# Performance work log

Measured on AMD Instinct MI355X. Metric: run time of the kernel, lower is better.

The kernel has to match this reference:

```python
import jax, jax.numpy as jnp
import numpy as np

N_HEAD, D_MODEL, D_K, D_V = 16, 1024, 64, 64
B, S = 2, 2048
LN_EPS = 1e-5


def setup_inputs() -> dict:
    key = jax.random.key(0)
    ks = jax.random.split(key, 9)
    std_qk = np.sqrt(2.0 / (D_MODEL + D_K)).astype(np.float32)
    std_v = np.sqrt(2.0 / (D_MODEL + D_V)).astype(np.float32)
    return {
        "q": jax.random.normal(ks[0], (B, S, D_MODEL), jnp.float32),
        "k": jax.random.normal(ks[1], (B, S, D_MODEL), jnp.float32),
        "v": jax.random.normal(ks[2], (B, S, D_MODEL), jnp.float32),
        # nn.Linear weights stored as [out, in]; we apply x @ W.T
        "w_qs": jax.random.normal(ks[3], (N_HEAD * D_K, D_MODEL), jnp.float32) * std_qk,
        "w_ks": jax.random.normal(ks[4], (N_HEAD * D_K, D_MODEL), jnp.float32) * std_qk,
        "w_vs": jax.random.normal(ks[5], (N_HEAD * D_V, D_MODEL), jnp.float32) * std_v,
        "fc_w": jax.random.normal(ks[6], (D_MODEL, N_HEAD * D_V), jnp.float32) * np.sqrt(2.0 / (D_MODEL + N_HEAD * D_V)).astype(np.float32),
        "fc_b": jnp.zeros((D_MODEL,), jnp.float32),
        "ln_g": jnp.ones((D_MODEL,), jnp.float32),
        "ln_b": jnp.zeros((D_MODEL,), jnp.float32),
    }


def reference(q, k, v, w_qs, w_ks, w_vs, fc_w, fc_b, ln_g, ln_b):
    temperature = jnp.asarray(np.power(D_K, 0.5), q.dtype)
    residual = q
    # projections -> [b, s, h, d]
    qh = (q @ w_qs.T).reshape(B, S, N_HEAD, D_K)
    kh = (k @ w_ks.T).reshape(B, S, N_HEAD, D_K)
    vh = (v @ w_vs.T).reshape(B, S, N_HEAD, D_V)
    # scaled dot-product attention (dropout = identity in eval)
    attn = jnp.einsum('bqhd,bkhd->bhqk', qh, kh) / temperature
    attn = jax.nn.softmax(attn, axis=-1)  # (log_softmax in source is unused)
    out = jnp.einsum('bhqk,bkhd->bqhd', attn, vh).reshape(B, S, N_HEAD * D_V)
    out = out @ fc_w.T + fc_b
    # layer norm over last dim
    x = out + residual
    mu = jnp.mean(x, axis=-1, keepdims=True)
    var = jnp.var(x, axis=-1, keepdims=True)
    return (x - mu) * jax.lax.rsqrt(var + LN_EPS) * ln_g + ln_b
```

## Files before the change

kernel.cpp:

```cpp
#include <hip/hip_runtime.h>
#include <hip/hip_bf16.h>

typedef _Float16 f16x8 __attribute__((ext_vector_type(8)));
typedef _Float16 f16x4 __attribute__((ext_vector_type(4)));
typedef _Float16 f16x2 __attribute__((ext_vector_type(2)));
typedef float f32x4 __attribute__((ext_vector_type(4)));

#define DEVI __device__ __forceinline__

constexpr int S_LEN = 2048;
constexpr int DM    = 1024;
constexpr int NH    = 16;
constexpr int DHD   = 64;
constexpr int MTOT  = 2 * S_LEN;

DEVI f32x4 mfma16(f16x8 a, f16x8 b, f32x4 c) {
    return __builtin_amdgcn_mfma_f32_16x16x32_f16(a, b, c, 0, 0, 0);
}

DEVI f16x2 cvt_pk(float a, float b) {
    return __builtin_bit_cast(f16x2, __builtin_amdgcn_cvt_pkrtz(a, b));
}

DEVI float fexp2(float x) {
#if __has_builtin(__builtin_amdgcn_exp2f)
    return __builtin_amdgcn_exp2f(x);
#else
    return exp2f(x);
#endif
}

__global__ void k_conv(const float* __restrict__ s0, const float* __restrict__ s1,
                       const float* __restrict__ s2, const float* __restrict__ s3,
                       const float* __restrict__ s4, const float* __restrict__ s5,
                       const float* __restrict__ s6,
                       _Float16* __restrict__ d0, _Float16* __restrict__ d1,
                       _Float16* __restrict__ d2, _Float16* __restrict__ d3,
                       _Float16* __restrict__ d4, _Float16* __restrict__ d5,
                       _Float16* __restrict__ d6)
{
    const int QN4 = (MTOT * DM) / 4;
    const int WN4 = (DM * DM) / 4;
    const int TOT = 3 * QN4 + 4 * WN4;
    int stride = gridDim.x * blockDim.x;
    for (int i = blockIdx.x * blockDim.x + threadIdx.x; i < TOT; i += stride) {
        const float* s; _Float16* d; int off;
        if (i < 3 * QN4) {
            int t = i / QN4; off = i - t * QN4;
            s = t == 0 ? s0 : (t == 1 ? s1 : s2);
            d = t == 0 ? d0 : (t == 1 ? d1 : d2);
        } else {
            int j = i - 3 * QN4;
            int t = j / WN4; off = j - t * WN4;
            s = t == 0 ? s3 : (t == 1 ? s4 : (t == 2 ? s5 : s6));
            d = t == 0 ? d3 : (t == 1 ? d4 : (t == 2 ? d5 : d6));
        }
        float4 v = reinterpret_cast<const float4*>(s)[off];
        f16x4 o;
        o[0] = (_Float16)v.x; o[1] = (_Float16)v.y;
        o[2] = (_Float16)v.z; o[3] = (_Float16)v.w;
        *reinterpret_cast<f16x4*>(d + (size_t)off * 4) = o;
    }
}

DEVI void gemm_main(const _Float16* __restrict__ A, const _Float16* __restrict__ Bw,
                    int kLen, int ld, int m0, int n0,
                    _Float16* As, _Float16* Bs, f32x4 (&acc)[4][4])
{
    const int tid = threadIdx.x;
    const int lane = tid & 63;
    const int w = tid >> 6;
    const int wm = w >> 1, wn = w & 1;
    const int lrow = lane & 15, lg = lane >> 4;
    const int srow = lane >> 3;
    const int sslot = lane & 7;

#pragma unroll
    for (int i = 0; i < 4; i++)
#pragma unroll
        for (int j = 0; j < 4; j++) acc[i][j] = f32x4{0.f, 0.f, 0.f, 0.f};

    f16x8 ra[4], rb[4];
#pragma unroll
    for (int q = 0; q < 4; q++) {
        int row = w * 8 + srow + q * 32;
        ra[q] = *reinterpret_cast<const f16x8*>(A  + (size_t)(m0 + row) * ld + sslot * 8);
        rb[q] = *reinterpret_cast<const f16x8*>(Bw + (size_t)(n0 + row) * ld + sslot * 8);
    }

    const int kTiles = kLen >> 6;
    for (int kt = 0; kt < kTiles; ++kt) {
        __syncthreads();
#pragma unroll
        for (int q = 0; q < 4; q++) {
            int row = w * 8 + srow + q * 32;
            int slot = sslot ^ (row & 7);
            *reinterpret_cast<f16x8*>(As + row * 64 + slot * 8) = ra[q];
            *reinterpret_cast<f16x8*>(Bs + row * 64 + slot * 8) = rb[q];
        }
        __syncthreads();
        if (kt + 1 < kTiles) {
#pragma unroll
            for (int q = 0; q < 4; q++) {
                int row = w * 8 + srow + q * 32;
                ra[q] = *reinterpret_cast<const f16x8*>(A  + (size_t)(m0 + row) * ld + (kt + 1) * 64 + sslot * 8);
                rb[q] = *reinterpret_cast<const f16x8*>(Bw + (size_t)(n0 + row) * ld + (kt + 1) * 64 + sslot * 8);
            }
        }
#pragma unroll
        for (int kk = 0; kk < 2; kk++) {
            f16x8 af[4], bfm[4];
#pragma unroll
            for (int i = 0; i < 4; i++) {
                int row = wm * 64 + i * 16 + lrow;
                int slot = (kk * 4 + lg) ^ (row & 7);
                af[i] = *reinterpret_cast<const f16x8*>(As + row * 64 + slot * 8);
            }
#pragma unroll
            for (int j = 0; j < 4; j++) {
                int row = wn * 64 + j * 16 + lrow;
                int slot = (kk * 4 + lg) ^ (row & 7);
                bfm[j] = *reinterpret_cast<const f16x8*>(Bs + row * 64 + slot * 8);
            }
#pragma unroll
            for (int i = 0; i < 4; i++)
#pragma unroll
                for (int j = 0; j < 4; j++)
                    acc[i][j] = mfma16(af[i], bfm[j], acc[i][j]);
        }
    }
}

__global__ __launch_bounds__(256, 2)
void k_proj(const _Float16* __restrict__ qb, const _Float16* __restrict__ kb,
            const _Float16* __restrict__ vb,
            const _Float16* __restrict__ wq, const _Float16* __restrict__ wk,
            const _Float16* __restrict__ wv,
            _Float16* __restrict__ Qh, _Float16* __restrict__ Kh, _Float16* __restrict__ Vt)
{
    __shared__ __align__(16) _Float16 As[128 * 64];
    __shared__ __align__(16) _Float16 Bs[128 * 64];
    const int z = blockIdx.z;
    const _Float16* A = z == 0 ? qb : (z == 1 ? kb : vb);
    const _Float16* B = z == 0 ? wq : (z == 1 ? wk : wv);
    const int m0 = blockIdx.x * 128, n0 = blockIdx.y * 128;
    f32x4 acc[4][4];
    gemm_main(A, B, DM, DM, m0, n0, As, Bs, acc);

    const int lane = threadIdx.x & 63, w = threadIdx.x >> 6;
    const int wm = w >> 1, wn = w & 1;
    const int lrow = lane & 15, lg = lane >> 4;

    if (z < 2) {
        _Float16* O = z == 0 ? Qh : Kh;
        const float scale = (z == 0) ? 0.18033688011112042f : 1.0f;
#pragma unroll
        for (int i = 0; i < 4; i++)
#pragma unroll
            for (int j = 0; j < 4; j++) {
                int n = n0 + wn * 64 + j * 16 + lrow;
                int h = n >> 6, d = n & 63;
#pragma unroll
                for (int r = 0; r < 4; r++) {
                    int m = m0 + wm * 64 + i * 16 + lg * 4 + r;
                    int b = m >> 11, s = m & (S_LEN - 1);
                    size_t idx = ((size_t)(b * NH + h) * S_LEN + s) * DHD + d;
                    O[idx] = (_Float16)(acc[i][j][r] * scale);
                }
            }
    } else {
#pragma unroll
        for (int i = 0; i < 4; i++) {
            int m = m0 + wm * 64 + i * 16 + lg * 4;
            int b = m >> 11, s = m & (S_LEN - 1);
#pragma unroll
            for (int j = 0; j < 4; j++) {
                int n = n0 + wn * 64 + j * 16 + lrow;
                int h = n >> 6, d = n & 63;
                size_t idx = ((size_t)(b * NH + h) * DHD + d) * S_LEN + s;
                f16x4 pk;
#pragma unroll
                for (int r = 0; r < 4; r++) pk[r] = (_Float16)acc[i][j][r];
                *reinterpret_cast<f16x4*>(Vt + idx) = pk;
            }
        }
    }
}

__global__ __launch_bounds__(256, 4)
void k_attn(const _Float16* __restrict__ Q, const _Float16* __restrict__ Kh,
            const _Float16* __restrict__ Vt, _Float16* __restrict__ Ob)
{
    __shared__ __align__(16) _Float16 Kl[2][64 * 64];
    __shared__ __align__(16) _Float16 Vl[2][64 * 64];
    __shared__ __align__(16) _Float16 Pl[4][16 * 64];

    const int tid  = threadIdx.x;
    const int lane = tid & 63, w = tid >> 6;
    const int lrow = lane & 15, lg = lane >> 4;

    const int raw  = blockIdx.x;
    const int swz  = (raw & 7) * 128 + (raw >> 3);
    const int bh   = swz >> 5;
    const int qblk = swz & 31;
    const int q0   = qblk * 64 + w * 16;

    const _Float16* Qb = Q  + (size_t)bh * S_LEN * DHD;
    const _Float16* Kb = Kh + (size_t)bh * S_LEN * DHD;
    const _Float16* Vb = Vt + (size_t)bh * DHD * S_LEN;

    f16x8 qf[2];
#pragma unroll
    for (int ks = 0; ks < 2; ks++)
        qf[ks] = *reinterpret_cast<const f16x8*>(Qb + (size_t)(q0 + lrow) * DHD + ks * 32 + lg * 8);

    f32x4 oacc[4];
#pragma unroll
    for (int df = 0; df < 4; df++) oacc[df] = f32x4{0.f, 0.f, 0.f, 0.f};
    f32x4 lacc = f32x4{0.f, 0.f, 0.f, 0.f};

    f16x8 vones;
#pragma unroll
    for (int i = 0; i < 8; i++) vones[i] = (_Float16)1.0f;

    const int srow8 = lane >> 3, sslot = lane & 7;
    const _Float16* gK = Kb + (size_t)(w * 16 + srow8) * DHD   + sslot * 8;
    const _Float16* gV = Vb + (size_t)(w * 16 + srow8) * S_LEN + sslot * 8;
    const int lds_st = (w * 16 + srow8) * 64 + (sslot ^ srow8) * 8;

    f16x8 stK[2], stV[2];
#pragma unroll
    for (int i = 0; i < 2; i++) {
        stK[i] = *reinterpret_cast<const f16x8*>(gK + i * 8 * DHD);
        stV[i] = *reinterpret_cast<const f16x8*>(gV + i * 8 * S_LEN);
    }

    for (int t = 0; t < 32; ++t) {
        const int cur = t & 1;
        _Float16* Kc = Kl[cur];
        _Float16* Vc = Vl[cur];
#pragma unroll
        for (int i = 0; i < 2; i++) {
            *reinterpret_cast<f16x8*>(Kc + lds_st + i * 8 * 64) = stK[i];
            *reinterpret_cast<f16x8*>(Vc + lds_st + i * 8 * 64) = stV[i];
        }
        if (t + 1 < 32) {
#pragma unroll
            for (int i = 0; i < 2; i++) {
                stK[i] = *reinterpret_cast<const f16x8*>(gK + (size_t)(t + 1) * 64 * DHD + i * 8 * DHD);
                stV[i] = *reinterpret_cast<const f16x8*>(gV + (t + 1) * 64 + i * 8 * S_LEN);
            }
        }
        asm volatile("s_waitcnt lgkmcnt(0)" ::: "memory");
        __builtin_amdgcn_s_barrier();

#pragma unroll
        for (int kf = 0; kf < 4; kf++) {
            const int r = kf * 16 + lrow;
            f16x8 k0 = *reinterpret_cast<const f16x8*>(Kc + r * 64 + ((lg    ) ^ (r & 7)) * 8);
            f16x8 k1 = *reinterpret_cast<const f16x8*>(Kc + r * 64 + ((4 + lg) ^ (r & 7)) * 8);
            __builtin_amdgcn_s_setprio(1);
            f32x4 sc = mfma16(k0, qf[0], f32x4{-7.f, -7.f, -7.f, -7.f});
            sc = mfma16(k1, qf[1], sc);
            __builtin_amdgcn_s_setprio(0);
            float p0 = fexp2(sc[0]), p1 = fexp2(sc[1]);
            float p2 = fexp2(sc[2]), p3 = fexp2(sc[3]);
            f16x4 hh = __builtin_shufflevector(cvt_pk(p0, p1), cvt_pk(p2, p3), 0, 1, 2, 3);
            const int sl = (kf * 2 + (lg >> 1)) ^ (lrow & 7);
            *reinterpret_cast<f16x4*>(&Pl[w][lrow * 64 + sl * 8 + (lg & 1) * 4]) = hh;
        }

#pragma unroll
        for (int ks = 0; ks < 2; ks++) {
            f16x8 pa = *reinterpret_cast<const f16x8*>(
                &Pl[w][lrow * 64 + ((ks * 4 + lg) ^ (lrow & 7)) * 8]);
            __builtin_amdgcn_s_setprio(1);
#pragma unroll
            for (int df = 0; df < 4; df++) {
                const int r = df * 16 + lrow;
                f16x8 vf = *reinterpret_cast<const f16x8*>(Vc + r * 64 + ((ks * 4 + lg) ^ (r & 7)) * 8);
                oacc[df] = mfma16(pa, vf, oacc[df]);
            }
            lacc = mfma16(pa, vones, lacc);
            __builtin_amdgcn_s_setprio(0);
        }
    }

    const int b = bh >> 4, h = bh & 15;
#pragma unroll
    for (int r = 0; r < 4; r++) {
        const float iq = 1.0f / lacc[r];
        const int m = b * S_LEN + q0 + lg * 4 + r;
#pragma unroll
        for (int df = 0; df < 4; df++)
            Ob[(size_t)m * DM + h * 64 + df * 16 + lrow] = (_Float16)(oacc[df][r] * iq);
    }
}

__global__ __launch_bounds__(256, 2)
void k_fc(const _Float16* __restrict__ Ob, const _Float16* __restrict__ Wfc,
          const float* __restrict__ bias,
          _Float16* __restrict__ fcoA, _Float16* __restrict__ fcoB)
{
    __shared__ __align__(16) _Float16 As[128 * 64];
    __shared__ __align__(16) _Float16 Bs[128 * 64];
    const int z = blockIdx.z;
    const int m0 = blockIdx.x * 128, n0 = blockIdx.y * 128;
    f32x4 acc[4][4];
    gemm_main(Ob + z * 512, Wfc + z * 512, 512, DM, m0, n0, As, Bs, acc);

    _Float16* out = z == 0 ? fcoA : fcoB;
    const int lane = threadIdx.x & 63, w = threadIdx.x >> 6;
    const int wm = w >> 1, wn = w & 1;
    const int lrow = lane & 15, lg = lane >> 4;
#pragma unroll
    for (int j = 0; j < 4; j++) {
        int n = n0 + wn * 64 + j * 16 + lrow;
        float bv = (z == 0) ? bias[n] : 0.f;
#pragma unroll
        for (int i = 0; i < 4; i++)
#pragma unroll
            for (int r = 0; r < 4; r++) {
                int m = m0 + wm * 64 + i * 16 + lg * 4 + r;
                out[(size_t)m * DM + n] = (_Float16)(acc[i][j][r] + bv);
            }
    }
}

__global__ void k_ln(const _Float16* __restrict__ fa, const _Float16* __restrict__ fb,
                     const float* __restrict__ res,
                     const float* __restrict__ g, const float* __restrict__ be,
                     float* __restrict__ out)
{
    int row = blockIdx.x * 4 + (threadIdx.x >> 6);
    int lane = threadIdx.x & 63;
    const f16x4* ar = reinterpret_cast<const f16x4*>(fa + (size_t)row * DM);
    const f16x4* br2 = reinterpret_cast<const f16x4*>(fb + (size_t)row * DM);
    const float4* rr = reinterpret_cast<const float4*>(res + (size_t)row * DM);
    float4 v[4];
    float sum = 0.f, sq = 0.f;
#pragma unroll
    for (int t = 0; t < 4; t++) {
        f16x4 a = ar[lane + 64 * t];
        f16x4 bq = br2[lane + 64 * t];
        float4 b = rr[lane + 64 * t];
        float4 c = make_float4((float)a[0] + (float)bq[0] + b.x,
                               (float)a[1] + (float)bq[1] + b.y,
                               (float)a[2] + (float)bq[2] + b.z,
                               (float)a[3] + (float)bq[3] + b.w);
        v[t] = c;
        sum += c.x + c.y + c.z + c.w;
        sq  += c.x * c.x + c.y * c.y + c.z * c.z + c.w * c.w;
    }
#pragma unroll
    for (int o = 1; o < 64; o <<= 1) { sum += __shfl_xor(sum, o); sq += __shfl_xor(sq, o); }
    float mu = sum * (1.f / DM);
    float rstd = rsqrtf(fmaxf(sq * (1.f / DM) - mu * mu, 0.f) + 1e-5f);
    float4* orow = reinterpret_cast<float4*>(out + (size_t)row * DM);
    const float4* gr = reinterpret_cast<const float4*>(g);
    const float4* brr = reinterpret_cast<const float4*>(be);
#pragma unroll
    for (int t = 0; t < 4; t++) {
        float4 gg = gr[lane + 64 * t], bb = brr[lane + 64 * t];
        float4 c = v[t];
        orow[lane + 64 * t] = make_float4((c.x - mu) * rstd * gg.x + bb.x,
                                          (c.y - mu) * rstd * gg.y + bb.y,
                                          (c.z - mu) * rstd * gg.z + bb.z,
                                          (c.w - mu) * rstd * gg.w + bb.w);
    }
}

extern "C" void kernel_launch(void* const* d_in, const int* in_sizes, int n_in,
                              void* d_out, int out_size, void* d_ws, size_t ws_size,
                              hipStream_t stream)
{
    const float* q    = (const float*)d_in[0];
    const float* k    = (const float*)d_in[1];
    const float* v    = (const float*)d_in[2];
    const float* w_qs = (const float*)d_in[3];
    const float* w_ks = (const float*)d_in[4];
    const float* w_vs = (const float*)d_in[5];
    const float* fc_w = (const float*)d_in[6];
    const float* fc_b = (const float*)d_in[7];
    const float* ln_g = (const float*)d_in[8];
    const float* ln_b = (const float*)d_in[9];
    float* out = (float*)d_out;

    if (ws_size < (size_t)67108864) return;

    _Float16* ws  = (_Float16*)d_ws;
    _Float16* qbf = ws;
    _Float16* kbf = qbf + 4194304;
    _Float16* vbf = kbf + 4194304;
    _Float16* wq  = vbf + 4194304;
    _Float16* wk  = wq + 1048576;
    _Float16* wv  = wk + 1048576;
    _Float16* wfc = wv + 1048576;
    _Float16* Qh  = wfc + 1048576;
    _Float16* Kh  = Qh + 4194304;
    _Float16* Vt  = Kh + 4194304;
    _Float16* Ob  = Vt + 4194304;
    _Float16* fcoA = qbf;
    _Float16* fcoB = kbf;

    k_conv<<<2048, 256, 0, stream>>>(q, k, v, w_qs, w_ks, w_vs, fc_w,
                                     qbf, kbf, vbf, wq, wk, wv, wfc);
    k_proj<<<dim3(32, 8, 3), 256, 0, stream>>>(qbf, kbf, vbf, wq, wk, wv, Qh, Kh, Vt);
    k_attn<<<1024, 256, 0, stream>>>(Qh, Kh, Vt, Ob);
    k_fc<<<dim3(32, 8, 2), 256, 0, stream>>>(Ob, wfc, fc_b, fcoA, fcoB);
    k_ln<<<1024, 256, 0, stream>>>(fcoA, fcoB, q, ln_g, ln_b, out);
}
```

Before: 134.1 us.

## Use direct global-to-LDS double-buffered GEMM loads and 32-row attention tiles per wave

The shared GEMM routine now loads tiles straight from global memory into LDS with global_load_lds, double-buffered, so it needs one barrier per k-step instead of staging through registers with two barriers. The XOR swizzle moves to the global address side. Attention now has each wave handle 32 query rows instead of 16, so every loaded K/V fragment feeds twice as many MFMAs. To fit this, the grid is halved and the occupancy hint is lowered. The changes add LDS and register pressure and rely on the barrier to wait for the async LDS loads to finish.

```diff
diff --git a/kernel.cpp b/kernel.cpp
--- a/kernel.cpp
+++ b/kernel.cpp
@@ -28,6 +28,12 @@
 #else
     return exp2f(x);
 #endif
+}
+
+DEVI void gload_lds16(const _Float16* g, _Float16* l) {
+    __builtin_amdgcn_global_load_lds(
+        (const __attribute__((address_space(1))) void*)g,
+        (__attribute__((address_space(3))) void*)l, 16, 0, 0);
 }
 
 __global__ void k_conv(const float* __restrict__ s0, const float* __restrict__ s1,
@@ -64,49 +70,47 @@
 }
 
 DEVI void gemm_main(const _Float16* __restrict__ A, const _Float16* __restrict__ Bw,
-                    int kLen, int ld, int m0, int n0,
-                    _Float16* As, _Float16* Bs, f32x4 (&acc)[4][4])
-{
+                    int kLen, int ld, int m0, int n0, f32x4 (&acc)[4][4])
+{
+    __shared__ __align__(16) _Float16 As[2][128 * 64];
+    __shared__ __align__(16) _Float16 Bs[2][128 * 64];
+
     const int tid = threadIdx.x;
     const int lane = tid & 63;
     const int w = tid >> 6;
     const int wm = w >> 1, wn = w & 1;
     const int lrow = lane & 15, lg = lane >> 4;
-    const int srow = lane >> 3;
-    const int sslot = lane & 7;
+    const int srow = w * 8 + (lane >> 3);
+    const int scol = ((lane & 7) ^ (srow & 7)) * 8;
 
 #pragma unroll
     for (int i = 0; i < 4; i++)
 #pragma unroll
         for (int j = 0; j < 4; j++) acc[i][j] = f32x4{0.f, 0.f, 0.f, 0.f};
 
-    f16x8 ra[4], rb[4];
+    const _Float16* gA = A  + (size_t)(m0 + srow) * ld + scol;
+    const _Float16* gB = Bw + (size_t)(n0 + srow) * ld + scol;
+
 #pragma unroll
     for (int q = 0; q < 4; q++) {
-        int row = w * 8 + srow + q * 32;
-        ra[q] = *reinterpret_cast<const f16x8*>(A  + (size_t)(m0 + row) * ld + sslot * 8);
-        rb[q] = *reinterpret_cast<const f16x8*>(Bw + (size_t)(n0 + row) * ld + sslot * 8);
+        gload_lds16(gA + (size_t)q * 32 * ld, &As[0][(w * 8 + q * 32) * 64]);
+        gload_lds16(gB + (size_t)q * 32 * ld, &Bs[0][(w * 8 + q * 32) * 64]);
     }
 
     const int kTiles = kLen >> 6;
     for (int kt = 0; kt < kTiles; ++kt) {
         __syncthreads();
-#pragma unroll
-        for (int q = 0; q < 4; q++) {
-            int row = w * 8 + srow + q * 32;
-            int slot = sslot ^ (row & 7);
-            *reinterpret_cast<f16x8*>(As + row * 64 + slot * 8) = ra[q];
-            *reinterpret_cast<f16x8*>(Bs + row * 64 + slot * 8) = rb[q];
-        }
-        __syncthreads();
         if (kt + 1 < kTiles) {
+            const int nb = (kt + 1) & 1;
+            const int ko = (kt + 1) * 64;
 #pragma unroll
             for (int q = 0; q < 4; q++) {
-                int row = w * 8 + srow + q * 32;
-                ra[q] = *reinterpret_cast<const f16x8*>(A  + (size_t)(m0 + row) * ld + (kt + 1) * 64 + sslot * 8);
-                rb[q] = *reinterpret_cast<const f16x8*>(Bw + (size_t)(n0 + row) * ld + (kt + 1) * 64 + sslot * 8);
-            }
-        }
+                gload_lds16(gA + ko + (size_t)q * 32 * ld, &As[nb][(w * 8 + q * 32) * 64]);
+                gload_lds16(gB + ko + (size_t)q * 32 * ld, &Bs[nb][(w * 8 + q * 32) * 64]);
+            }
+        }
+        const _Float16* Ab = As[kt & 1];
+        const _Float16* Bb = Bs[kt & 1];
 #pragma unroll
         for (int kk = 0; kk < 2; kk++) {
             f16x8 af[4], bfm[4];
@@ -114,13 +118,13 @@
             for (int i = 0; i < 4; i++) {
                 int row = wm * 64 + i * 16 + lrow;
                 int slot = (kk * 4 + lg) ^ (row & 7);
-                af[i] = *reinterpret_cast<const f16x8*>(As + row * 64 + slot * 8);
+                af[i] = *reinterpret_cast<const f16x8*>(Ab + row * 64 + slot * 8);
             }
 #pragma unroll
             for (int j = 0; j < 4; j++) {
                 int row = wn * 64 + j * 16 + lrow;
                 int slot = (kk * 4 + lg) ^ (row & 7);
-                bfm[j] = *reinterpret_cast<const f16x8*>(Bs + row * 64 + slot * 8);
+                bfm[j] = *reinterpret_cast<const f16x8*>(Bb + row * 64 + slot * 8);
             }
 #pragma unroll
             for (int i = 0; i < 4; i++)
@@ -138,14 +142,12 @@
             const _Float16* __restrict__ wv,
             _Float16* __restrict__ Qh, _Float16* __restrict__ Kh, _Float16* __restrict__ Vt)
 {
-    __shared__ __align__(16) _Float16 As[128 * 64];
-    __shared__ __align__(16) _Float16 Bs[128 * 64];
     const int z = blockIdx.z;
     const _Float16* A = z == 0 ? qb : (z == 1 ? kb : vb);
     const _Float16* B = z == 0 ? wq : (z == 1 ? wk : wv);
     const int m0 = blockIdx.x * 128, n0 = blockIdx.y * 128;
     f32x4 acc[4][4];
-    gemm_main(A, B, DM, DM, m0, n0, As, Bs, acc);
+    gemm_main(A, B, DM, DM, m0, n0, acc);
 
     const int lane = threadIdx.x & 63, w = threadIdx.x >> 6;
     const int wm = w >> 1, wn = w & 1;
@@ -187,37 +189,42 @@
     }
 }
 
-__global__ __launch_bounds__(256, 4)
+__global__ __launch_bounds__(256, 2)
 void k_attn(const _Float16* __restrict__ Q, const _Float16* __restrict__ Kh,
             const _Float16* __restrict__ Vt, _Float16* __restrict__ Ob)
 {
     __shared__ __align__(16) _Float16 Kl[2][64 * 64];
     __shared__ __align__(16) _Float16 Vl[2][64 * 64];
-    __shared__ __align__(16) _Float16 Pl[4][16 * 64];
+    __shared__ __align__(16) _Float16 Pl[4][32 * 64];
 
     const int tid  = threadIdx.x;
     const int lane = tid & 63, w = tid >> 6;
     const int lrow = lane & 15, lg = lane >> 4;
 
     const int raw  = blockIdx.x;
-    const int swz  = (raw & 7) * 128 + (raw >> 3);
-    const int bh   = swz >> 5;
-    const int qblk = swz & 31;
-    const int q0   = qblk * 64 + w * 16;
+    const int swz  = (raw & 7) * 64 + (raw >> 3);
+    const int bh   = swz >> 4;
+    const int qblk = swz & 15;
+    const int q0   = qblk * 128 + w * 32;
 
     const _Float16* Qb = Q  + (size_t)bh * S_LEN * DHD;
     const _Float16* Kb = Kh + (size_t)bh * S_LEN * DHD;
     const _Float16* Vb = Vt + (size_t)bh * DHD * S_LEN;
 
-    f16x8 qf[2];
-#pragma unroll
-    for (int ks = 0; ks < 2; ks++)
-        qf[ks] = *reinterpret_cast<const f16x8*>(Qb + (size_t)(q0 + lrow) * DHD + ks * 32 + lg * 8);
-
-    f32x4 oacc[4];
-#pragma unroll
-    for (int df = 0; df < 4; df++) oacc[df] = f32x4{0.f, 0.f, 0.f, 0.f};
-    f32x4 lacc = f32x4{0.f, 0.f, 0.f, 0.f};
+    f16x8 qf[2][2];
+#pragma unroll
+    for (int mi = 0; mi < 2; mi++)
+#pragma unroll
+        for (int ks = 0; ks < 2; ks++)
+            qf[mi][ks] = *reinterpret_cast<const f16x8*>(
+                Qb + (size_t)(q0 + mi * 16 + lrow) * DHD + ks * 32 + lg * 8);
+
+    f32x4 oacc[2][4];
+#pragma unroll
+    for (int mi = 0; mi < 2; mi++)
+#pragma unroll
+        for (int df = 0; df < 4; df++) oacc[mi][df] = f32x4{0.f, 0.f, 0.f, 0.f};
+    f32x4 lacc[2] = {f32x4{0.f, 0.f, 0.f, 0.f}, f32x4{0.f, 0.f, 0.f, 0.f}};
 
     f16x8 vones;
 #pragma unroll
@@ -260,41 +267,56 @@
             f16x8 k0 = *reinterpret_cast<const f16x8*>(Kc + r * 64 + ((lg    ) ^ (r & 7)) * 8);
             f16x8 k1 = *reinterpret_cast<const f16x8*>(Kc + r * 64 + ((4 + lg) ^ (r & 7)) * 8);
             __builtin_amdgcn_s_setprio(1);
-            f32x4 sc = mfma16(k0, qf[0], f32x4{-7.f, -7.f, -7.f, -7.f});
-            sc = mfma16(k1, qf[1], sc);
+            f32x4 sc0 = mfma16(k0, qf[0][0], f32x4{-7.f, -7.f, -7.f, -7.f});
+            sc0 = mfma16(k1, qf[0][1], sc0);
+            f32x4 sc1 = mfma16(k0, qf[1][0], f32x4{-7.f, -7.f, -7.f, -7.f});
+            sc1 = mfma16(k1, qf[1][1], sc1);
             __builtin_amdgcn_s_setprio(0);
-            float p0 = fexp2(sc[0]), p1 = fexp2(sc[1]);
-            float p2 = fexp2(sc[2]), p3 = fexp2(sc[3]);
-            f16x4 hh = __builtin_shufflevector(cvt_pk(p0, p1), cvt_pk(p2, p3), 0, 1, 2, 3);
             const int sl = (kf * 2 + (lg >> 1)) ^ (lrow & 7);
-            *reinterpret_cast<f16x4*>(&Pl[w][lrow * 64 + sl * 8 + (lg & 1) * 4]) = hh;
+            {
+                float p0 = fexp2(sc0[0]), p1 = fexp2(sc0[1]);
+                float p2 = fexp2(sc0[2]), p3 = fexp2(sc0[3]);
+                f16x4 hh = __builtin_shufflevector(cvt_pk(p0, p1), cvt_pk(p2, p3), 0, 1, 2, 3);
+                *reinterpret_cast<f16x4*>(&Pl[w][lrow * 64 + sl * 8 + (lg & 1) * 4]) = hh;
+            }
+            {
+                float p0 = fexp2(sc1[0]), p1 = fexp2(sc1[1]);
+                float p2 = fexp2(sc1[2]), p3 = fexp2(sc1[3]);
+                f16x4 hh = __builtin_shufflevector(cvt_pk(p0, p1), cvt_pk(p2, p3), 0, 1, 2, 3);
+                *reinterpret_cast<f16x4*>(&Pl[w][(16 + lrow) * 64 + sl * 8 + (lg & 1) * 4]) = hh;
+            }
         }
 
 #pragma unroll
         for (int ks = 0; ks < 2; ks++) {
-            f16x8 pa = *reinterpret_cast<const f16x8*>(
-                &Pl[w][lrow * 64 + ((ks * 4 + lg) ^ (lrow & 7)) * 8]);
+            const int psl = ((ks * 4 + lg) ^ (lrow & 7)) * 8;
+            f16x8 pa0 = *reinterpret_cast<const f16x8*>(&Pl[w][lrow * 64 + psl]);
+            f16x8 pa1 = *reinterpret_cast<const f16x8*>(&Pl[w][(16 + lrow) * 64 + psl]);
             __builtin_amdgcn_s_setprio(1);
 #pragma unroll
             for (int df = 0; df < 4; df++) {
                 const int r = df * 16 + lrow;
                 f16x8 vf = *reinterpret_cast<const f16x8*>(Vc + r * 64 + ((ks * 4 + lg) ^ (r & 7)) * 8);
-                oacc[df] = mfma16(pa, vf, oacc[df]);
-            }
-            lacc = mfma16(pa, vones, lacc);
+                oacc[0][df] = mfma16(pa0, vf, oacc[0][df]);
+                oacc[1][df] = mfma16(pa1, vf, oacc[1][df]);
+            }
+            lacc[0] = mfma16(pa0, vones, lacc[0]);
+            lacc[1] = mfma16(pa1, vones, lacc[1]);
             __builtin_amdgcn_s_setprio(0);
         }
     }
 
     const int b = bh >> 4, h = bh & 15;
 #pragma unroll
-    for (int r = 0; r < 4; r++) {
-        const float iq = 1.0f / lacc[r];
-        const int m = b * S_LEN + q0 + lg * 4 + r;
-#pragma unroll
-        for (int df = 0; df < 4; df++)
-            Ob[(size_t)m * DM + h * 64 + df * 16 + lrow] = (_Float16)(oacc[df][r] * iq);
-    }
+    for (int mi = 0; mi < 2; mi++)
+#pragma unroll
+        for (int r = 0; r < 4; r++) {
+            const float iq = 1.0f / lacc[mi][r];
+            const int m = b * S_LEN + q0 + mi * 16 + lg * 4 + r;
+#pragma unroll
+            for (int df = 0; df < 4; df++)
+                Ob[(size_t)m * DM + h * 64 + df * 16 + lrow] = (_Float16)(oacc[mi][df][r] * iq);
+        }
 }
 
 __global__ __launch_bounds__(256, 2)
@@ -302,12 +324,10 @@
           const float* __restrict__ bias,
           _Float16* __restrict__ fcoA, _Float16* __restrict__ fcoB)
 {
-    __shared__ __align__(16) _Float16 As[128 * 64];
-    __shared__ __align__(16) _Float16 Bs[128 * 64];
     const int z = blockIdx.z;
     const int m0 = blockIdx.x * 128, n0 = blockIdx.y * 128;
     f32x4 acc[4][4];
-    gemm_main(Ob + z * 512, Wfc + z * 512, 512, DM, m0, n0, As, Bs, acc);
+    gemm_main(Ob + z * 512, Wfc + z * 512, 512, DM, m0, n0, acc);
 
     _Float16* out = z == 0 ? fcoA : fcoB;
     const int lane = threadIdx.x & 63, w = threadIdx.x >> 6;
@@ -406,7 +426,7 @@
     k_conv<<<2048, 256, 0, stream>>>(q, k, v, w_qs, w_ks, w_vs, fc_w,
                                      qbf, kbf, vbf, wq, wk, wv, wfc);
     k_proj<<<dim3(32, 8, 3), 256, 0, stream>>>(qbf, kbf, vbf, wq, wk, wv, Qh, Kh, Vt);
-    k_attn<<<1024, 256, 0, stream>>>(Qh, Kh, Vt, Ob);
+    k_attn<<<512, 256, 0, stream>>>(Qh, Kh, Vt, Ob);
     k_fc<<<dim3(32, 8, 2), 256, 0, stream>>>(Ob, wfc, fc_b, fcoA, fcoB);
     k_ln<<<1024, 256, 0, stream>>>(fcoA, fcoB, q, ln_g, ln_b, out);
 }
```

Result: no change. 133.5 us (-0.4%).
